# Kernel optimization log

Measured on AMD Instinct MI355X. Metric: run time of the kernel, lower is better.

## Reference

```python
import jax, jax.numpy as jnp
import numpy as np

B, T, E = 2, 4096, 1024
H = 16
D = E // H  # head_len = 64


def setup_inputs() -> dict:
    key = jax.random.key(0)
    ks = jax.random.split(key, 6)
    s = 1.0 / np.sqrt(E)
    return {
        "x": jax.random.normal(ks[0], (B, T, E), dtype=jnp.float32),
        # torch nn.Linear weights: shape (out, in), y = x @ W.T
        "Wq": jax.random.uniform(ks[1], (E, E), jnp.float32, -s, s),
        "Wk": jax.random.uniform(ks[2], (E, E), jnp.float32, -s, s),
        "Wv": jax.random.uniform(ks[3], (E, E), jnp.float32, -s, s),
        "Wo": jax.random.uniform(ks[4], (E, E), jnp.float32, -s, s),
        "bo": jax.random.uniform(ks[5], (E,), jnp.float32, -s, s),
    }


def reference(x, Wq, Wk, Wv, Wo, bo):
    Bx, Tx, Ex = x.shape
    q = x @ Wq.T
    k = x @ Wk.T
    v = x @ Wv.T
    # (B, T, H, D) -> (B, H, T, D)
    q = q.reshape(Bx, Tx, H, D).transpose(0, 2, 1, 3)
    k = k.reshape(Bx, Tx, H, D).transpose(0, 2, 1, 3)
    v = v.reshape(Bx, Tx, H, D).transpose(0, 2, 1, 3)
    # scores: (B, H, T, T), scaled by sqrt(head_len)
    sim = jnp.einsum("bhqd,bhkd->bhqk", q, k) / jnp.sqrt(jnp.float32(D))
    causal = jnp.tril(jnp.ones((Tx, Tx), dtype=bool))  # True = keep
    sim = jnp.where(causal[None, None], sim, -jnp.inf)
    attn = jax.nn.softmax(sim, axis=-1)
    # dropout_rate = 0.0 (eval) -> identity
    out = jnp.einsum("bhqk,bhkd->bhqd", attn, v)
    out = out.transpose(0, 2, 1, 3).reshape(Bx, Tx, Ex)
    return out @ Wo.T + bo
```

## Files before the change

### kernel.cpp

```cpp
#include <hip/hip_runtime.h>

typedef unsigned short bf16_t;
typedef __bf16 bf16x8 __attribute__((ext_vector_type(8)));
typedef float  v4f   __attribute__((ext_vector_type(4)));
typedef float  v16f  __attribute__((ext_vector_type(16)));
typedef unsigned u32x2 __attribute__((ext_vector_type(2)));

__device__ __forceinline__ bf16_t f2bf(float f) {
    union { float f; unsigned u; } a; a.f = f;
    unsigned r = a.u + 0x7FFFu + ((a.u >> 16) & 1u);
    return (bf16_t)(r >> 16);
}

__device__ __forceinline__ unsigned cvtpk(float lo, float hi) {
    unsigned r;
    asm("v_cvt_pk_bf16_f32 %0, %1, %2" : "=v"(r) : "v"(lo), "v"(hi));
    return r;
}

__device__ __forceinline__ v16f zero16() {
    v16f z;
#pragma unroll
    for (int i = 0; i < 16; ++i) z[i] = 0.f;
    return z;
}

#define GL16(g, l) __builtin_amdgcn_global_load_lds( \
    (__attribute__((address_space(1))) void*)(g),    \
    (__attribute__((address_space(3))) void*)(l), 16, 0, 0)

#define QSCALE 0.18033688011f

__global__ __launch_bounds__(256) void cvt_all(
    const float4* __restrict__ x,  const float4* __restrict__ wq,
    const float4* __restrict__ wk, const float4* __restrict__ wv,
    const float4* __restrict__ wo,
    ushort4* __restrict__ xb, ushort4* __restrict__ wqkv, ushort4* __restrict__ wob) {
    int i = blockIdx.x * 256 + threadIdx.x;
    const float4* s; ushort4* d; int off;
    if (i < 2097152) { s = x; d = xb; off = i; }
    else {
        int wdx = (i - 2097152) >> 18;
        off = (i - 2097152) & 262143;
        if      (wdx == 0) { s = wq; d = wqkv; }
        else if (wdx == 1) { s = wk; d = wqkv + 262144; }
        else if (wdx == 2) { s = wv; d = wqkv + 524288; }
        else               { s = wo; d = wob; }
    }
    float4 v = s[off];
    ushort4 o;
    o.x = f2bf(v.x); o.y = f2bf(v.y); o.z = f2bf(v.z); o.w = f2bf(v.w);
    d[off] = o;
}

#define GEMM_MAINLOOP(A_, W_)                                                          \
    __shared__ bf16_t SMEM[8192];                                                      \
    bf16_t* As = SMEM; bf16_t* Bs = SMEM + 4096;                                       \
    const int tid = threadIdx.x;                                                       \
    const int w = tid >> 6, lane = tid & 63;                                           \
    const int lrow = lane & 15, lq = lane >> 4;                                        \
    const int nwg_ = gridDim.x * gridDim.y;                                            \
    const int id_ = blockIdx.y * gridDim.x + blockIdx.x;                               \
    const int sid_ = (id_ & 7) * (nwg_ >> 3) + (id_ >> 3);                             \
    const int bxs = sid_ % gridDim.x, bys = sid_ / gridDim.x;                          \
    const int m0 = bys * 128, n0 = bxs * 128;                                          \
    const int srow = w * 16 + (lane >> 2);                                             \
    const int sk = (lane & 3) * 8;                                                     \
    const int wm = (w & 1) * 64, wn = (w >> 1) * 64;                                   \
    v4f acc[4][4];                                                                     \
    _Pragma("unroll") for (int i = 0; i < 4; ++i)                                      \
        _Pragma("unroll") for (int j = 0; j < 4; ++j)                                  \
            acc[i][j] = (v4f){0.f, 0.f, 0.f, 0.f};                                     \
    for (int k0 = 0; k0 < 1024; k0 += 32) {                                            \
        __syncthreads();                                                               \
        GL16(A_ + (size_t)(m0 + srow) * 1024 + k0 + sk,      (char*)As + w * 1024);    \
        GL16(A_ + (size_t)(m0 + 64 + srow) * 1024 + k0 + sk, (char*)As + 4096 + w * 1024); \
        GL16(W_ + (size_t)(n0 + srow) * 1024 + k0 + sk,      (char*)Bs + w * 1024);    \
        GL16(W_ + (size_t)(n0 + 64 + srow) * 1024 + k0 + sk, (char*)Bs + 4096 + w * 1024); \
        __syncthreads();                                                               \
        bf16x8 af[4], bf[4];                                                           \
        _Pragma("unroll") for (int i = 0; i < 4; ++i)                                  \
            af[i] = *(const bf16x8*)&As[(wm + i * 16 + lrow) * 32 + lq * 8];           \
        _Pragma("unroll") for (int j = 0; j < 4; ++j)                                  \
            bf[j] = *(const bf16x8*)&Bs[(wn + j * 16 + lrow) * 32 + lq * 8];           \
        _Pragma("unroll") for (int i = 0; i < 4; ++i)                                  \
            _Pragma("unroll") for (int j = 0; j < 4; ++j)                              \
                acc[i][j] = __builtin_amdgcn_mfma_f32_16x16x32_bf16(af[i], bf[j],      \
                                                                    acc[i][j], 0, 0, 0); \
    }

__global__ __launch_bounds__(256) void gemm_qkv_kernel(
    const bf16_t* __restrict__ A, const bf16_t* __restrict__ W,
    bf16_t* __restrict__ Qb, bf16_t* __restrict__ Kb, bf16_t* __restrict__ Vtb) {
    GEMM_MAINLOOP(A, W)
    const int x = bxs;
    const int b = m0 >> 12, t0 = m0 & 4095;
    if (x < 8) {
#pragma unroll
        for (int i = 0; i < 4; ++i)
#pragma unroll
            for (int j = 0; j < 4; ++j)
#pragma unroll
                for (int r = 0; r < 4; ++r) {
                    int t = t0 + wm + i * 16 + lq * 4 + r;
                    int n = n0 + wn + j * 16 + lrow;
                    int h = n >> 6, d = n & 63;
                    Qb[(((size_t)b * 16 + h) * 4096 + t) * 64 + d] =
                        f2bf(acc[i][j][r] * QSCALE);
                }
    } else if (x < 16) {
#pragma unroll
        for (int i = 0; i < 4; ++i)
#pragma unroll
            for (int j = 0; j < 4; ++j)
#pragma unroll
                for (int r = 0; r < 4; ++r) {
                    int t = t0 + wm + i * 16 + lq * 4 + r;
                    int nn = n0 + wn + j * 16 + lrow - 1024;
                    int h = nn >> 6, d = nn & 63;
                    Kb[(((size_t)b * 16 + h) * 4096 + t) * 64 + d] = f2bf(acc[i][j][r]);
                }
    } else {
        const int d0 = n0 - 2048;
#pragma unroll 1
        for (int p = 0; p < 2; ++p) {
            __syncthreads();
            if ((w >> 1) == p) {
#pragma unroll
                for (int i = 0; i < 4; ++i)
#pragma unroll
                    for (int j = 0; j < 4; ++j) {
                        int row = j * 16 + lrow;
                        int swz = (row & 7) << 1;
                        int g = (wm >> 2) + i * 4 + lq;
                        uint2 u;
                        u.x = (unsigned)f2bf(acc[i][j][0]) | ((unsigned)f2bf(acc[i][j][1]) << 16);
                        u.y = (unsigned)f2bf(acc[i][j][2]) | ((unsigned)f2bf(acc[i][j][3]) << 16);
                        *(uint2*)&SMEM[row * 128 + ((g ^ swz) << 2)] = u;
                    }
            }
            __syncthreads();
#pragma unroll
            for (int uu = 0; uu < 4; ++uu) {
                int unit = tid + 256 * uu;
                int row = unit >> 4, seg = unit & 15;
                uint4 val = *(const uint4*)&SMEM[row * 128 + ((seg ^ (row & 7)) << 3)];
                *(uint4*)&Vtb[((size_t)b * 1024 + d0 + p * 64 + row) * 4096 + t0 + seg * 8] = val;
            }
        }
    }
}

__global__ __launch_bounds__(256) void gemm_out_kernel(
    const bf16_t* __restrict__ A, const bf16_t* __restrict__ W,
    const float* __restrict__ bo, float* __restrict__ out) {
    GEMM_MAINLOOP(A, W)
#pragma unroll
    for (int j = 0; j < 4; ++j) {
        int n = n0 + wn + j * 16 + lrow;
        float bias = bo[n];
#pragma unroll
        for (int i = 0; i < 4; ++i)
#pragma unroll
            for (int r = 0; r < 4; ++r) {
                int m = m0 + wm + i * 16 + lq * 4 + r;
                out[(size_t)m * 1024 + n] = acc[i][j][r] + bias;
            }
    }
}

__global__ __launch_bounds__(256, 2) void attn_kernel(
    const bf16_t* __restrict__ Q, const bf16_t* __restrict__ K,
    const bf16_t* __restrict__ Vt, bf16_t* __restrict__ O) {
    __shared__ bf16_t Kls[2][64 * 64];
    __shared__ bf16_t Vls[2][64 * 64];
    const int tid = threadIdx.x;
    const int w = tid >> 6, lane = tid & 63;
    const int l31 = lane & 31, lh = lane >> 5;
    const int bh = blockIdx.y;
    const int g = blockIdx.x;

    const bf16_t* Qh = Q + (size_t)bh * (4096 * 64);
    const bf16_t* Kh = K + (size_t)bh * (4096 * 64);
    const bf16_t* Vh = Vt + (size_t)bh * (64 * 4096);
    const int b = bh >> 4, h = bh & 15;

    const int svrow = lane >> 3;
    const int sg8 = ((lane & 7) ^ svrow) * 8;
    const int rx = l31 & 7;

    bf16x8 ones;
#pragma unroll
    for (int i = 0; i < 8; ++i) ones[i] = (__bf16)1.0f;

#pragma unroll 1
    for (int mem = 0; mem < 2; ++mem) {
        const int j = mem ? (31 - g) : g;
        const int q0 = j * 128;
        const int q0w = q0 + w * 32;
        const int nt = 2 * j + 2;
        const int wlast = 2 * j + (w >> 1);
        const int qglob = q0w + l31;

        bf16x8 qf[4];
#pragma unroll
        for (int dk = 0; dk < 4; ++dk)
            qf[dk] = *(const bf16x8*)&Qh[(size_t)(q0w + l31) * 64 + dk * 16 + lh * 8];

        v16f oacc0 = zero16(), oacc1 = zero16(), lacc = zero16();

        auto stage = [&](int kt, int buf) {
            const int kc0 = kt << 6;
#pragma unroll
            for (int i = 0; i < 2; ++i) {
                int r0 = w * 16 + i * 8;
                GL16(Kh + (size_t)(kc0 + r0 + svrow) * 64 + sg8, (char*)&Kls[buf][r0 * 64]);
                GL16(Vh + (size_t)(r0 + svrow) * 4096 + kc0 + sg8, (char*)&Vls[buf][r0 * 64]);
            }
        };

        stage(0, 0);
        for (int kt = 0; kt < nt; ++kt) {
            const int buf = kt & 1;
            __syncthreads();
            if (kt + 1 < nt) stage(kt + 1, buf ^ 1);
            if (kt > wlast) continue;
            const int kc0 = kt << 6;
            const bool diag = (kt == wlast);

            bf16x8 kf[2][4];
#pragma unroll
            for (int th = 0; th < 2; ++th)
#pragma unroll
                for (int dk = 0; dk < 4; ++dk)
                    kf[th][dk] = *(const bf16x8*)
                        &Kls[buf][(th * 32 + l31) * 64 + (((dk * 2 + lh) ^ rx) * 8)];
            bf16x8 vf[2][4];
#pragma unroll
            for (int db = 0; db < 2; ++db)
#pragma unroll
                for (int kb = 0; kb < 4; ++kb)
                    vf[db][kb] = *(const bf16x8*)
                        &Vls[buf][(db * 32 + l31) * 64 + (((kb * 2 + lh) ^ rx) * 8)];

            v16f st0 = zero16(), st1 = zero16();
            __builtin_amdgcn_s_setprio(1);
#pragma unroll
            for (int dk = 0; dk < 4; ++dk) {
                st0 = __builtin_amdgcn_mfma_f32_32x32x16_bf16(kf[0][dk], qf[dk], st0, 0, 0, 0);
                st1 = __builtin_amdgcn_mfma_f32_32x32x16_bf16(kf[1][dk], qf[dk], st1, 0, 0, 0);
            }
            __builtin_amdgcn_s_setprio(0);

            bf16x8 pa[4];
#pragma unroll
            for (int th = 0; th < 2; ++th) {
                float p[16];
#pragma unroll
                for (int rr = 0; rr < 16; ++rr) {
                    float pv = __builtin_amdgcn_exp2f(th ? st1[rr] : st0[rr]);
                    if (diag) {
                        int tg = kc0 + th * 32 + (rr & 3) + 8 * (rr >> 2) + 4 * lh;
                        pv = (tg > qglob) ? 0.f : pv;
                    }
                    p[rr] = pv;
                }
#pragma unroll
                for (int kb2 = 0; kb2 < 2; ++kb2) {
                    unsigned x0 = cvtpk(p[kb2 * 8 + 0], p[kb2 * 8 + 1]);
                    unsigned x1 = cvtpk(p[kb2 * 8 + 2], p[kb2 * 8 + 3]);
                    unsigned y0 = cvtpk(p[kb2 * 8 + 4], p[kb2 * 8 + 5]);
                    unsigned y1 = cvtpk(p[kb2 * 8 + 6], p[kb2 * 8 + 7]);
                    u32x2 ra = __builtin_amdgcn_permlane32_swap(x0, y0, false, false);
                    u32x2 rb = __builtin_amdgcn_permlane32_swap(x1, y1, false, false);
                    union { unsigned u[4]; bf16x8 v; } pu;
                    pu.u[0] = ra.x; pu.u[1] = rb.x;
                    pu.u[2] = ra.y; pu.u[3] = rb.y;
                    pa[th * 2 + kb2] = pu.v;
                }
            }

            __builtin_amdgcn_s_setprio(1);
#pragma unroll
            for (int kb = 0; kb < 4; ++kb) {
                lacc  = __builtin_amdgcn_mfma_f32_32x32x16_bf16(pa[kb], ones,       lacc,  0, 0, 0);
                oacc0 = __builtin_amdgcn_mfma_f32_32x32x16_bf16(pa[kb], vf[0][kb], oacc0, 0, 0, 0);
                oacc1 = __builtin_amdgcn_mfma_f32_32x32x16_bf16(pa[kb], vf[1][kb], oacc1, 0, 0, 0);
            }
            __builtin_amdgcn_s_setprio(0);
        }

#pragma unroll
        for (int rr = 0; rr < 16; ++rr) {
            float rl = 1.0f / lacc[rr];
            int q = q0w + (rr & 3) + 8 * (rr >> 2) + 4 * lh;
            size_t o0 = ((size_t)b * 4096 + q) * 1024 + h * 64;
            O[o0 + l31]      = f2bf(oacc0[rr] * rl);
            O[o0 + 32 + l31] = f2bf(oacc1[rr] * rl);
        }
    }
}

extern "C" void kernel_launch(void* const* d_in, const int* in_sizes, int n_in,
                              void* d_out, int out_size, void* d_ws, size_t ws_size,
                              hipStream_t stream) {
    const float* x  = (const float*)d_in[0];
    const float* Wq = (const float*)d_in[1];
    const float* Wk = (const float*)d_in[2];
    const float* Wv = (const float*)d_in[3];
    const float* Wo = (const float*)d_in[4];
    const float* bo = (const float*)d_in[5];
    float* out = (float*)d_out;

    char* ws = (char*)d_ws;
    bf16_t* xb   = (bf16_t*)(ws + 0);
    bf16_t* Wqkv = (bf16_t*)(ws + 16777216);
    bf16_t* Wob  = (bf16_t*)(ws + 23068672);
    bf16_t* Qb   = (bf16_t*)(ws + 25165824);
    bf16_t* Kb   = (bf16_t*)(ws + 41943040);
    bf16_t* Vtb  = (bf16_t*)(ws + 58720256);
    bf16_t* Ob   = (bf16_t*)(ws + 75497472);

    cvt_all<<<12288, 256, 0, stream>>>((const float4*)x, (const float4*)Wq,
                                       (const float4*)Wk, (const float4*)Wv,
                                       (const float4*)Wo,
                                       (ushort4*)xb, (ushort4*)Wqkv, (ushort4*)Wob);

    gemm_qkv_kernel<<<dim3(24, 64), 256, 0, stream>>>(xb, Wqkv, Qb, Kb, Vtb);

    attn_kernel<<<dim3(16, 32), 256, 0, stream>>>(Qb, Kb, Vtb, Ob);

    gemm_out_kernel<<<dim3(8, 64), 256, 0, stream>>>(Ob, Wob, bo, out);
}
```

Baseline: 311.0 us.

## Swap MFMA operands for vectorized GEMM epilogues, remap attention grid, drop setprio

The GEMM mainloop is split into setup and k-loop macros, with an option to swap the MFMA A/B operands. With the swap, each lane holds four consecutive output columns, so the Q/K epilogues and the output projection can write packed 8-byte bf16 and 16-byte float4 stores instead of scalar scattered stores, and the bias is read with float4 loads. The attention kernel remaps block IDs so that eight consecutive blocks share a query-tile index across different heads, which changes the scheduling order and cache locality. It also removes the s_setprio hints around the MFMA sections, which changes wave scheduling priority and could hurt latency hiding.

```diff
diff --git a/kernel.cpp b/kernel.cpp
--- a/kernel.cpp
+++ b/kernel.cpp
@@ -53,7 +53,7 @@
     d[off] = o;
 }
 
-#define GEMM_MAINLOOP(A_, W_)                                                          \
+#define GEMM_SETUP                                                                     \
     __shared__ bf16_t SMEM[8192];                                                      \
     bf16_t* As = SMEM; bf16_t* Bs = SMEM + 4096;                                       \
     const int tid = threadIdx.x;                                                       \
@@ -70,7 +70,9 @@
     v4f acc[4][4];                                                                     \
     _Pragma("unroll") for (int i = 0; i < 4; ++i)                                      \
         _Pragma("unroll") for (int j = 0; j < 4; ++j)                                  \
-            acc[i][j] = (v4f){0.f, 0.f, 0.f, 0.f};                                     \
+            acc[i][j] = (v4f){0.f, 0.f, 0.f, 0.f};
+
+#define GEMM_KLOOP(A_, W_, SWAP)                                                       \
     for (int k0 = 0; k0 < 1024; k0 += 32) {                                            \
         __syncthreads();                                                               \
         GL16(A_ + (size_t)(m0 + srow) * 1024 + k0 + sk,      (char*)As + w * 1024);    \
@@ -85,42 +87,52 @@
             bf[j] = *(const bf16x8*)&Bs[(wn + j * 16 + lrow) * 32 + lq * 8];           \
         _Pragma("unroll") for (int i = 0; i < 4; ++i)                                  \
             _Pragma("unroll") for (int j = 0; j < 4; ++j)                              \
-                acc[i][j] = __builtin_amdgcn_mfma_f32_16x16x32_bf16(af[i], bf[j],      \
-                                                                    acc[i][j], 0, 0, 0); \
+                acc[i][j] = (SWAP)                                                     \
+                    ? __builtin_amdgcn_mfma_f32_16x16x32_bf16(bf[j], af[i], acc[i][j], 0, 0, 0) \
+                    : __builtin_amdgcn_mfma_f32_16x16x32_bf16(af[i], bf[j], acc[i][j], 0, 0, 0); \
     }
 
 __global__ __launch_bounds__(256) void gemm_qkv_kernel(
     const bf16_t* __restrict__ A, const bf16_t* __restrict__ W,
     bf16_t* __restrict__ Qb, bf16_t* __restrict__ Kb, bf16_t* __restrict__ Vtb) {
-    GEMM_MAINLOOP(A, W)
+    GEMM_SETUP
     const int x = bxs;
     const int b = m0 >> 12, t0 = m0 & 4095;
-    if (x < 8) {
-#pragma unroll
-        for (int i = 0; i < 4; ++i)
-#pragma unroll
-            for (int j = 0; j < 4; ++j)
-#pragma unroll
-                for (int r = 0; r < 4; ++r) {
-                    int t = t0 + wm + i * 16 + lq * 4 + r;
-                    int n = n0 + wn + j * 16 + lrow;
+    if (x < 16) {
+        GEMM_KLOOP(A, W, 1)
+        if (x < 8) {
+#pragma unroll
+            for (int i = 0; i < 4; ++i) {
+                int t = t0 + wm + i * 16 + lrow;
+#pragma unroll
+                for (int j = 0; j < 4; ++j) {
+                    int n = n0 + wn + j * 16 + lq * 4;
                     int h = n >> 6, d = n & 63;
-                    Qb[(((size_t)b * 16 + h) * 4096 + t) * 64 + d] =
-                        f2bf(acc[i][j][r] * QSCALE);
+                    uint2 u;
+                    u.x = (unsigned)f2bf(acc[i][j][0] * QSCALE) |
+                          ((unsigned)f2bf(acc[i][j][1] * QSCALE) << 16);
+                    u.y = (unsigned)f2bf(acc[i][j][2] * QSCALE) |
+                          ((unsigned)f2bf(acc[i][j][3] * QSCALE) << 16);
+                    *(uint2*)&Qb[(((size_t)b * 16 + h) * 4096 + t) * 64 + d] = u;
                 }
-    } else if (x < 16) {
-#pragma unroll
-        for (int i = 0; i < 4; ++i)
-#pragma unroll
-            for (int j = 0; j < 4; ++j)
-#pragma unroll
-                for (int r = 0; r < 4; ++r) {
-                    int t = t0 + wm + i * 16 + lq * 4 + r;
-                    int nn = n0 + wn + j * 16 + lrow - 1024;
+            }
+        } else {
+#pragma unroll
+            for (int i = 0; i < 4; ++i) {
+                int t = t0 + wm + i * 16 + lrow;
+#pragma unroll
+                for (int j = 0; j < 4; ++j) {
+                    int nn = n0 + wn + j * 16 + lq * 4 - 1024;
                     int h = nn >> 6, d = nn & 63;
-                    Kb[(((size_t)b * 16 + h) * 4096 + t) * 64 + d] = f2bf(acc[i][j][r]);
+                    uint2 u;
+                    u.x = (unsigned)f2bf(acc[i][j][0]) | ((unsigned)f2bf(acc[i][j][1]) << 16);
+                    u.y = (unsigned)f2bf(acc[i][j][2]) | ((unsigned)f2bf(acc[i][j][3]) << 16);
+                    *(uint2*)&Kb[(((size_t)b * 16 + h) * 4096 + t) * 64 + d] = u;
                 }
+            }
+        }
     } else {
+        GEMM_KLOOP(A, W, 0)
         const int d0 = n0 - 2048;
 #pragma unroll 1
         for (int p = 0; p < 2; ++p) {
@@ -154,18 +166,20 @@
 __global__ __launch_bounds__(256) void gemm_out_kernel(
     const bf16_t* __restrict__ A, const bf16_t* __restrict__ W,
     const float* __restrict__ bo, float* __restrict__ out) {
-    GEMM_MAINLOOP(A, W)
+    GEMM_SETUP
+    GEMM_KLOOP(A, W, 1)
 #pragma unroll
     for (int j = 0; j < 4; ++j) {
-        int n = n0 + wn + j * 16 + lrow;
-        float bias = bo[n];
-#pragma unroll
-        for (int i = 0; i < 4; ++i)
-#pragma unroll
-            for (int r = 0; r < 4; ++r) {
-                int m = m0 + wm + i * 16 + lq * 4 + r;
-                out[(size_t)m * 1024 + n] = acc[i][j][r] + bias;
-            }
+        int nb = n0 + wn + j * 16 + lq * 4;
+        float4 bv = *(const float4*)&bo[nb];
+#pragma unroll
+        for (int i = 0; i < 4; ++i) {
+            int m = m0 + wm + i * 16 + lrow;
+            float4 o;
+            o.x = acc[i][j][0] + bv.x; o.y = acc[i][j][1] + bv.y;
+            o.z = acc[i][j][2] + bv.z; o.w = acc[i][j][3] + bv.w;
+            *(float4*)&out[(size_t)m * 1024 + nb] = o;
+        }
     }
 }
 
@@ -177,8 +191,10 @@
     const int tid = threadIdx.x;
     const int w = tid >> 6, lane = tid & 63;
     const int l31 = lane & 31, lh = lane >> 5;
-    const int bh = blockIdx.y;
-    const int g = blockIdx.x;
+
+    const int id = blockIdx.y * 16 + blockIdx.x;
+    const int g = (id >> 3) & 15;
+    const int bh = (id & 7) + ((id >> 7) << 3);
 
     const bf16_t* Qh = Q + (size_t)bh * (4096 * 64);
     const bf16_t* Kh = K + (size_t)bh * (4096 * 64);
@@ -244,13 +260,11 @@
                         &Vls[buf][(db * 32 + l31) * 64 + (((kb * 2 + lh) ^ rx) * 8)];
 
             v16f st0 = zero16(), st1 = zero16();
-            __builtin_amdgcn_s_setprio(1);
 #pragma unroll
             for (int dk = 0; dk < 4; ++dk) {
                 st0 = __builtin_amdgcn_mfma_f32_32x32x16_bf16(kf[0][dk], qf[dk], st0, 0, 0, 0);
                 st1 = __builtin_amdgcn_mfma_f32_32x32x16_bf16(kf[1][dk], qf[dk], st1, 0, 0, 0);
             }
-            __builtin_amdgcn_s_setprio(0);
 
             bf16x8 pa[4];
 #pragma unroll
@@ -280,14 +294,12 @@
                 }
             }
 
-            __builtin_amdgcn_s_setprio(1);
 #pragma unroll
             for (int kb = 0; kb < 4; ++kb) {
                 lacc  = __builtin_amdgcn_mfma_f32_32x32x16_bf16(pa[kb], ones,       lacc,  0, 0, 0);
                 oacc0 = __builtin_amdgcn_mfma_f32_32x32x16_bf16(pa[kb], vf[0][kb], oacc0, 0, 0, 0);
                 oacc1 = __builtin_amdgcn_mfma_f32_32x32x16_bf16(pa[kb], vf[1][kb], oacc1, 0, 0, 0);
             }
-            __builtin_amdgcn_s_setprio(0);
         }
 
 #pragma unroll
```

After: 305.4 us. About the same (-1.8%).
